# Performance work log

Measured on AMD Instinct MI355X. Metric: run time of the kernel, lower is better.

The kernel has to match this reference:

```python
import jax, jax.numpy as jnp
import numpy as np

B, N, T, D, H = 8, 1000, 64, 32, 4
HD = D // H
GEN_INTERVAL = 5.0


def setup_inputs() -> dict:
    key = jax.random.key(0)
    ks = jax.random.split(key, 10)
    s = 1.0 / np.sqrt(D)
    inp = {
        "x": jax.random.normal(ks[0], (B, N, T, D), dtype=jnp.float32),
        "q_w": jax.random.uniform(ks[1], (D, D), jnp.float32, -s, s),
        "q_b": jnp.zeros((D,), jnp.float32),
        "k_w": jax.random.uniform(ks[2], (D, D), jnp.float32, -s, s),
        "k_b": jnp.zeros((D,), jnp.float32),
        "v_w": jax.random.uniform(ks[3], (D, D), jnp.float32, -s, s),
        "v_b": jnp.zeros((D,), jnp.float32),
        "out_w": jax.random.uniform(ks[4], (D, D), jnp.float32, -s, s),
        "out_b": jnp.zeros((D,), jnp.float32),
        "rel_pos_bias": jax.random.uniform(ks[5], (H, T, T), jnp.float32, -s, s),
        "log_gi": jnp.array(np.log(GEN_INTERVAL), jnp.float32),
    }
    return inp


def _gi_mask(log_gi, t):
    # generation-interval weighting: gaussian around gen_int + recency term, causal
    gen_int = jnp.exp(log_gi)
    times = jnp.arange(t, dtype=jnp.float32)
    lag = times[:, None] - times[None, :]  # [T, T]
    weight = jnp.exp(-0.5 * ((lag - gen_int) / (gen_int * 0.5)) ** 2)
    recent = jnp.exp(-0.1 * jnp.abs(lag))
    mask = 0.7 * weight + 0.3 * recent
    causal = jnp.tril(jnp.ones((t, t), jnp.float32))
    return mask * causal


def reference(x, q_w, q_b, k_w, k_b, v_w, v_b, out_w, out_b, rel_pos_bias, log_gi):
    b, n, t, d = x.shape
    xf = x.reshape(b * n, t, d)
    q = (xf @ q_w + q_b).reshape(b * n, t, H, HD).transpose(0, 2, 1, 3)  # [BN,H,T,hd]
    k = (xf @ k_w + k_b).reshape(b * n, t, H, HD).transpose(0, 2, 1, 3)
    v = (xf @ v_w + v_b).reshape(b * n, t, H, HD).transpose(0, 2, 1, 3)
    scale = jnp.sqrt(jnp.asarray(HD, jnp.float32))
    attn = jnp.einsum("bhqd,bhkd->bhqk", q, k) / scale  # [BN,H,T,T]
    attn = attn + rel_pos_bias[None]
    gi = _gi_mask(log_gi, t)
    attn = attn * gi[None, None]
    attn = jax.nn.softmax(attn, axis=-1)
    out = jnp.einsum("bhqk,bhkd->bhqd", attn, v)
    out = out.transpose(0, 2, 1, 3).reshape(b * n, t, d)
    out = out @ out_w + out_b
    return out.reshape(b, n, t, d)
```

## Files before the change

kernel.cpp:

```cpp
#include <hip/hip_runtime.h>
#include <math.h>

namespace {
constexpr int T_ = 64;
constexpr int D_ = 32;

typedef _Float16 half4 __attribute__((ext_vector_type(4)));
typedef _Float16 half8 __attribute__((ext_vector_type(8)));
typedef float f32x4 __attribute__((ext_vector_type(4)));

__global__ __launch_bounds__(256) void gia_prep(
    const float* __restrict__ qw, const float* __restrict__ kw,
    const float* __restrict__ vw, const float* __restrict__ ow,
    const float* __restrict__ rel, const float* __restrict__ lgi,
    _Float16* __restrict__ tbl, _Float16* __restrict__ wimg)
{
    int t = blockIdx.x * 256 + threadIdx.x;
    if (t < 4096) {
        const float gv = __expf(lgi[0]);
        const float LOG2E = 1.4426950408889634f;
        const float INVS  = 0.35355339059327373f;
        int h = t >> 10, nt = (t >> 8) & 3, mt = (t >> 6) & 3, lane = t & 63;
        int q  = (lane & 15) + 16 * nt;
        int k0 = 16 * mt + 4 * (lane >> 4);
        _Float16 vals[8];
#pragma unroll
        for (int r = 0; r < 4; ++r) {
            int k = k0 + r;
            float lag = (float)(q - k);
            float gi = 0.0f;
            if (k <= q) {
                float z = (lag - gv) / (0.5f * gv);
                gi = 0.7f * __expf(-0.5f * z * z) + 0.3f * __expf(-0.1f * lag);
            }
            vals[r]     = (_Float16)(gi * INVS * LOG2E);
            vals[4 + r] = (_Float16)(rel[(h * 64 + q) * 64 + k] * gi * LOG2E);
        }
#pragma unroll
        for (int i = 0; i < 8; ++i) tbl[t * 8 + i] = vals[i];
    } else if (t < 6656) {
        int wi = t - 4096;
        const float* wp[4] = {qw, kw, vw, ow};
#pragma unroll
        for (int e = 0; e < 2; ++e) {
            int flat = wi * 2 + e;
            int m = flat / 1280, rem = flat % 1280;
            int c2 = rem / 40, kk = rem % 40;
            float v = (kk < 32) ? wp[m][kk * 32 + c2] : 0.0f;
            wimg[flat] = (_Float16)v;
        }
    }
}

__global__ __launch_bounds__(256) void gia_main(
    const float* __restrict__ x,
    const float* __restrict__ qb_, const float* __restrict__ kb_,
    const float* __restrict__ vb_, const float* __restrict__ ob_,
    const _Float16* __restrict__ tbl, const _Float16* __restrict__ wimg,
    float* __restrict__ out)
{
    __shared__ __align__(16) _Float16 xs[64][40];
    __shared__ __align__(16) _Float16 wS[4][32][40];
    __shared__ __align__(16) _Float16 qs[64][36];
    __shared__ __align__(16) _Float16 ks_[64][36];
    __shared__ __align__(16) _Float16 vT[32][72];
    __shared__ __align__(16) _Float16 os_[64][40];
    __shared__ float bS[4][32];

    const int tid  = threadIdx.x;
    const int lane = tid & 63;
    const int w    = tid >> 6;
    const int l4   = lane & 15;
    const int g    = lane >> 4;
    const int bn   = blockIdx.x;

    {
        const float4* xv = (const float4*)(x + (size_t)bn * 2048);
        float4 a = xv[2 * tid], b = xv[2 * tid + 1];
        int t = tid >> 2, c = (tid & 3) * 8;
        half8 hx;
        hx[0] = (_Float16)a.x; hx[1] = (_Float16)a.y;
        hx[2] = (_Float16)a.z; hx[3] = (_Float16)a.w;
        hx[4] = (_Float16)b.x; hx[5] = (_Float16)b.y;
        hx[6] = (_Float16)b.z; hx[7] = (_Float16)b.w;
        *(half8*)&xs[t][c] = hx;

        const uint4* wsrc = (const uint4*)wimg;
        uint4* wdst = (uint4*)&wS[0][0][0];
        wdst[tid]        = wsrc[tid];
        wdst[tid + 256]  = wsrc[tid + 256];
        if (tid < 128) wdst[tid + 512] = wsrc[tid + 512];
        if (tid < 128) {
            int m = tid >> 5, i = tid & 31;
            const float* bp = (m == 0) ? qb_ : (m == 1) ? kb_ : (m == 2) ? vb_ : ob_;
            bS[m][i] = bp[i];
        }
    }
    __syncthreads();

    {
        half4 xa0 = *(const half4*)&xs[16 * w + l4][4 * g];
        half4 xa1 = *(const half4*)&xs[16 * w + l4][4 * g + 16];
#pragma unroll
        for (int m = 0; m < 3; ++m) {
#pragma unroll
            for (int nt = 0; nt < 2; ++nt) {
                half4 wb0 = *(const half4*)&wS[m][l4 + 16 * nt][4 * g];
                half4 wb1 = *(const half4*)&wS[m][l4 + 16 * nt][4 * g + 16];
                f32x4 acc = {};
                acc = __builtin_amdgcn_mfma_f32_16x16x16f16(xa0, wb0, acc, 0, 0, 0);
                acc = __builtin_amdgcn_mfma_f32_16x16x16f16(xa1, wb1, acc, 0, 0, 0);
                float bb = bS[m][l4 + 16 * nt];
                if (m == 0) {
#pragma unroll
                    for (int r = 0; r < 4; ++r)
                        qs[g * 4 + r + 16 * w][l4 + 16 * nt] = (_Float16)(acc[r] + bb);
                } else if (m == 1) {
#pragma unroll
                    for (int r = 0; r < 4; ++r)
                        ks_[g * 4 + r + 16 * w][l4 + 16 * nt] = (_Float16)(acc[r] + bb);
                } else {
                    half4 pv;
#pragma unroll
                    for (int r = 0; r < 4; ++r) pv[r] = (_Float16)(acc[r] + bb);
                    *(half4*)&vT[l4 + 16 * nt][g * 4 + 16 * w] = pv;
                }
            }
        }
    }
    __syncthreads();

    {
        const int h = w;
        half4 kfr[4], qfr[4], vfr[4];
#pragma unroll
        for (int mt = 0; mt < 4; ++mt) {
            half4 v = {};
            if (g < 2) v = *(const half4*)&ks_[l4 + 16 * mt][8 * h + 4 * g];
            kfr[mt] = v;
        }
#pragma unroll
        for (int nt = 0; nt < 4; ++nt) {
            half4 v = {};
            if (g < 2) v = *(const half4*)&qs[l4 + 16 * nt][8 * h + 4 * g];
            qfr[nt] = v;
        }
#pragma unroll
        for (int ks = 0; ks < 4; ++ks) {
            half4 v = {};
            if (l4 < 8) v = *(const half4*)&vT[8 * h + l4][4 * g + 16 * ks];
            vfr[ks] = v;
        }

        f32x4 oacc[4];
#pragma unroll
        for (int i = 0; i < 4; ++i) oacc[i] = (f32x4){};

        const half8* tbl8 = (const half8*)tbl;
#pragma unroll
        for (int nt = 0; nt < 4; ++nt) {
            half8 tb[4];
#pragma unroll
            for (int mt = 0; mt < 4; ++mt)
                tb[mt] = tbl8[((h * 4 + nt) * 4 + mt) * 64 + lane];
            f32x4 s[4];
#pragma unroll
            for (int mt = 0; mt < 4; ++mt) {
                f32x4 z = {};
                s[mt] = __builtin_amdgcn_mfma_f32_16x16x16f16(kfr[mt], qfr[nt], z, 0, 0, 0);
            }
            float p[16];
#pragma unroll
            for (int mt = 0; mt < 4; ++mt)
#pragma unroll
                for (int r = 0; r < 4; ++r)
                    p[mt * 4 + r] =
                        fmaf(s[mt][r], (float)tb[mt][r], (float)tb[mt][4 + r]);
            float mx = p[0];
#pragma unroll
            for (int i = 1; i < 16; ++i) mx = fmaxf(mx, p[i]);
            mx = fmaxf(mx, __shfl_xor(mx, 16));
            mx = fmaxf(mx, __shfl_xor(mx, 32));
            float sum = 0.0f;
#pragma unroll
            for (int i = 0; i < 16; ++i) {
                float e = exp2f(p[i] - mx);
                p[i] = e;
                sum += e;
            }
            sum += __shfl_xor(sum, 16);
            sum += __shfl_xor(sum, 32);
            float inv = 1.0f / sum;
#pragma unroll
            for (int ks = 0; ks < 4; ++ks) {
                half4 af;
                af[0] = (_Float16)(p[ks * 4 + 0] * inv);
                af[1] = (_Float16)(p[ks * 4 + 1] * inv);
                af[2] = (_Float16)(p[ks * 4 + 2] * inv);
                af[3] = (_Float16)(p[ks * 4 + 3] * inv);
                oacc[nt] = __builtin_amdgcn_mfma_f32_16x16x16f16(af, vfr[ks], oacc[nt], 0, 0, 0);
            }
        }
        if (l4 < 8) {
#pragma unroll
            for (int nt = 0; nt < 4; ++nt)
#pragma unroll
                for (int r = 0; r < 4; ++r)
                    os_[g * 4 + r + 16 * nt][8 * h + l4] = (_Float16)oacc[nt][r];
        }
    }
    __syncthreads();

    {
        half4 oa0 = *(const half4*)&os_[16 * w + l4][4 * g];
        half4 oa1 = *(const half4*)&os_[16 * w + l4][4 * g + 16];
        float* yout = out + (size_t)bn * 2048;
#pragma unroll
        for (int nt = 0; nt < 2; ++nt) {
            half4 wb0 = *(const half4*)&wS[3][l4 + 16 * nt][4 * g];
            half4 wb1 = *(const half4*)&wS[3][l4 + 16 * nt][4 * g + 16];
            f32x4 y = {};
            y = __builtin_amdgcn_mfma_f32_16x16x16f16(oa0, wb0, y, 0, 0, 0);
            y = __builtin_amdgcn_mfma_f32_16x16x16f16(oa1, wb1, y, 0, 0, 0);
            float bb = bS[3][l4 + 16 * nt];
#pragma unroll
            for (int r = 0; r < 4; ++r)
                yout[(g * 4 + r + 16 * w) * 32 + l4 + 16 * nt] = y[r] + bb;
        }
    }
}

}

extern "C" void kernel_launch(void* const* d_in, const int* in_sizes, int n_in,
                              void* d_out, int out_size, void* d_ws, size_t ws_size,
                              hipStream_t stream)
{
    const float* x   = (const float*)d_in[0];
    const float* qw  = (const float*)d_in[1];
    const float* qb  = (const float*)d_in[2];
    const float* kw  = (const float*)d_in[3];
    const float* kb  = (const float*)d_in[4];
    const float* vw  = (const float*)d_in[5];
    const float* vb  = (const float*)d_in[6];
    const float* ow  = (const float*)d_in[7];
    const float* ob  = (const float*)d_in[8];
    const float* rel = (const float*)d_in[9];
    const float* lgi = (const float*)d_in[10];
    float* outp = (float*)d_out;

    _Float16* tbl  = (_Float16*)d_ws;
    _Float16* wimg = tbl + 32768;

    const int bn_count = in_sizes[0] / (T_ * D_);

    gia_prep<<<dim3(26), dim3(256), 0, stream>>>(qw, kw, vw, ow, rel, lgi, tbl, wimg);
    gia_main<<<dim3(bn_count), dim3(256), 0, stream>>>(
        x, qb, kb, vb, ob, tbl, wimg, outp);
}
```

Baseline: 76.41 us.

## Factor softmax exponent, drop max subtraction, and get row sums from ones column

The softmax is rewritten without max subtraction. exp(s*g + b*g) is split into exp2 of the score times a per-position fp32 gate table, multiplied by a precomputed fp16 exp(bias*gate) table. A ones row is appended to each head's V slice so the PV MFMA also produces the row sum. Normalization is then applied to the head outputs just before the output projection. This removes the per-row max/sum shuffle reductions and the division inside the attention loop, and reuses the x buffer as the output staging area. The trade-off is possible fp16 overflow if scores grow large, since there is no max subtraction.

```diff
diff --git a/kernel.cpp b/kernel.cpp
--- a/kernel.cpp
+++ b/kernel.cpp
@@ -5,47 +5,63 @@
 constexpr int T_ = 64;
 constexpr int D_ = 32;
 
+typedef _Float16 half2 __attribute__((ext_vector_type(2)));
 typedef _Float16 half4 __attribute__((ext_vector_type(4)));
 typedef _Float16 half8 __attribute__((ext_vector_type(8)));
 typedef float f32x4 __attribute__((ext_vector_type(4)));
+
+union H4 { half4 v4; half2 v2[2]; };
 
 __global__ __launch_bounds__(256) void gia_prep(
     const float* __restrict__ qw, const float* __restrict__ kw,
     const float* __restrict__ vw, const float* __restrict__ ow,
     const float* __restrict__ rel, const float* __restrict__ lgi,
-    _Float16* __restrict__ tbl, _Float16* __restrict__ wimg)
+    float* __restrict__ gis32, _Float16* __restrict__ ebg,
+    _Float16* __restrict__ wimg)
 {
     int t = blockIdx.x * 256 + threadIdx.x;
-    if (t < 4096) {
-        const float gv = __expf(lgi[0]);
-        const float LOG2E = 1.4426950408889634f;
-        const float INVS  = 0.35355339059327373f;
-        int h = t >> 10, nt = (t >> 8) & 3, mt = (t >> 6) & 3, lane = t & 63;
+    const float gv = __expf(lgi[0]);
+    const float LOG2E = 1.4426950408889634f;
+    const float INVS  = 0.35355339059327373f;
+    if (t < 1024) {
+        int nt = t >> 8, mt = (t >> 6) & 3, lane = t & 63;
         int q  = (lane & 15) + 16 * nt;
         int k0 = 16 * mt + 4 * (lane >> 4);
-        _Float16 vals[8];
 #pragma unroll
         for (int r = 0; r < 4; ++r) {
             int k = k0 + r;
-            float lag = (float)(q - k);
             float gi = 0.0f;
             if (k <= q) {
+                float lag = (float)(q - k);
                 float z = (lag - gv) / (0.5f * gv);
                 gi = 0.7f * __expf(-0.5f * z * z) + 0.3f * __expf(-0.1f * lag);
             }
-            vals[r]     = (_Float16)(gi * INVS * LOG2E);
-            vals[4 + r] = (_Float16)(rel[(h * 64 + q) * 64 + k] * gi * LOG2E);
-        }
-#pragma unroll
-        for (int i = 0; i < 8; ++i) tbl[t * 8 + i] = vals[i];
-    } else if (t < 6656) {
-        int wi = t - 4096;
+            gis32[t * 4 + r] = gi * INVS * LOG2E;
+        }
+    } else if (t < 5120) {
+        int e = t - 1024;
+        int h = e >> 10, nt = (e >> 8) & 3, mt = (e >> 6) & 3, lane = e & 63;
+        int q  = (lane & 15) + 16 * nt;
+        int k0 = 16 * mt + 4 * (lane >> 4);
+#pragma unroll
+        for (int r = 0; r < 4; ++r) {
+            int k = k0 + r;
+            float gi = 0.0f;
+            if (k <= q) {
+                float lag = (float)(q - k);
+                float z = (lag - gv) / (0.5f * gv);
+                gi = 0.7f * __expf(-0.5f * z * z) + 0.3f * __expf(-0.1f * lag);
+            }
+            ebg[e * 4 + r] = (_Float16)__expf(rel[(h * 64 + q) * 64 + k] * gi);
+        }
+    } else if (t < 7424) {
+        int wi = t - 5120;
         const float* wp[4] = {qw, kw, vw, ow};
 #pragma unroll
         for (int e = 0; e < 2; ++e) {
             int flat = wi * 2 + e;
-            int m = flat / 1280, rem = flat % 1280;
-            int c2 = rem / 40, kk = rem % 40;
+            int m = flat / 1152, rem = flat % 1152;
+            int c2 = rem / 36, kk = rem % 36;
             float v = (kk < 32) ? wp[m][kk * 32 + c2] : 0.0f;
             wimg[flat] = (_Float16)v;
         }
@@ -56,16 +72,17 @@
     const float* __restrict__ x,
     const float* __restrict__ qb_, const float* __restrict__ kb_,
     const float* __restrict__ vb_, const float* __restrict__ ob_,
-    const _Float16* __restrict__ tbl, const _Float16* __restrict__ wimg,
+    const float* __restrict__ gis32, const _Float16* __restrict__ ebg,
+    const _Float16* __restrict__ wimg,
     float* __restrict__ out)
 {
     __shared__ __align__(16) _Float16 xs[64][40];
-    __shared__ __align__(16) _Float16 wS[4][32][40];
-    __shared__ __align__(16) _Float16 qs[64][36];
-    __shared__ __align__(16) _Float16 ks_[64][36];
-    __shared__ __align__(16) _Float16 vT[32][72];
-    __shared__ __align__(16) _Float16 os_[64][40];
+    __shared__ __align__(16) _Float16 wS[4][32][36];
+    __shared__ __align__(16) _Float16 qs[64][40];
+    __shared__ __align__(16) _Float16 ks_[64][40];
+    __shared__ __align__(16) _Float16 vT[37][72];
     __shared__ float bS[4][32];
+    __shared__ float invS[4][64];
 
     const int tid  = threadIdx.x;
     const int lane = tid & 63;
@@ -87,9 +104,15 @@
 
         const uint4* wsrc = (const uint4*)wimg;
         uint4* wdst = (uint4*)&wS[0][0][0];
-        wdst[tid]        = wsrc[tid];
-        wdst[tid + 256]  = wsrc[tid + 256];
-        if (tid < 128) wdst[tid + 512] = wsrc[tid + 512];
+        wdst[tid]       = wsrc[tid];
+        wdst[tid + 256] = wsrc[tid + 256];
+        if (tid < 64) wdst[tid + 512] = wsrc[tid + 512];
+
+        if (tid < 128) {
+            int h = tid >> 5, j = tid & 31;
+            half2 o2 = {(_Float16)1.0f, (_Float16)1.0f};
+            *(half2*)&vT[9 * h + 8][2 * j] = o2;
+        }
         if (tid < 128) {
             int m = tid >> 5, i = tid & 31;
             const float* bp = (m == 0) ? qb_ : (m == 1) ? kb_ : (m == 2) ? vb_ : ob_;
@@ -123,7 +146,8 @@
                     half4 pv;
 #pragma unroll
                     for (int r = 0; r < 4; ++r) pv[r] = (_Float16)(acc[r] + bb);
-                    *(half4*)&vT[l4 + 16 * nt][g * 4 + 16 * w] = pv;
+                    int c = l4 + 16 * nt;
+                    *(half4*)&vT[9 * (c >> 3) + (c & 7)][g * 4 + 16 * w] = pv;
                 }
             }
         }
@@ -145,75 +169,68 @@
             if (g < 2) v = *(const half4*)&qs[l4 + 16 * nt][8 * h + 4 * g];
             qfr[nt] = v;
         }
-#pragma unroll
-        for (int ks = 0; ks < 4; ++ks) {
-            half4 v = {};
-            if (l4 < 8) v = *(const half4*)&vT[8 * h + l4][4 * g + 16 * ks];
-            vfr[ks] = v;
-        }
+        const int vrow = 9 * h + (l4 < 9 ? l4 : 9);
+#pragma unroll
+        for (int ks = 0; ks < 4; ++ks)
+            vfr[ks] = *(const half4*)&vT[vrow][4 * g + 16 * ks];
 
         f32x4 oacc[4];
 #pragma unroll
         for (int i = 0; i < 4; ++i) oacc[i] = (f32x4){};
 
-        const half8* tbl8 = (const half8*)tbl;
 #pragma unroll
         for (int nt = 0; nt < 4; ++nt) {
-            half8 tb[4];
-#pragma unroll
-            for (int mt = 0; mt < 4; ++mt)
-                tb[mt] = tbl8[((h * 4 + nt) * 4 + mt) * 64 + lane];
             f32x4 s[4];
 #pragma unroll
             for (int mt = 0; mt < 4; ++mt) {
                 f32x4 z = {};
                 s[mt] = __builtin_amdgcn_mfma_f32_16x16x16f16(kfr[mt], qfr[nt], z, 0, 0, 0);
             }
-            float p[16];
-#pragma unroll
-            for (int mt = 0; mt < 4; ++mt)
-#pragma unroll
-                for (int r = 0; r < 4; ++r)
-                    p[mt * 4 + r] =
-                        fmaf(s[mt][r], (float)tb[mt][r], (float)tb[mt][4 + r]);
-            float mx = p[0];
-#pragma unroll
-            for (int i = 1; i < 16; ++i) mx = fmaxf(mx, p[i]);
-            mx = fmaxf(mx, __shfl_xor(mx, 16));
-            mx = fmaxf(mx, __shfl_xor(mx, 32));
-            float sum = 0.0f;
-#pragma unroll
-            for (int i = 0; i < 16; ++i) {
-                float e = exp2f(p[i] - mx);
-                p[i] = e;
-                sum += e;
-            }
-            sum += __shfl_xor(sum, 16);
-            sum += __shfl_xor(sum, 32);
-            float inv = 1.0f / sum;
-#pragma unroll
-            for (int ks = 0; ks < 4; ++ks) {
-                half4 af;
-                af[0] = (_Float16)(p[ks * 4 + 0] * inv);
-                af[1] = (_Float16)(p[ks * 4 + 1] * inv);
-                af[2] = (_Float16)(p[ks * 4 + 2] * inv);
-                af[3] = (_Float16)(p[ks * 4 + 3] * inv);
-                oacc[nt] = __builtin_amdgcn_mfma_f32_16x16x16f16(af, vfr[ks], oacc[nt], 0, 0, 0);
-            }
-        }
+            half4 af[4];
+#pragma unroll
+            for (int mt = 0; mt < 4; ++mt) {
+                f32x4 g4 = *(const f32x4*)&gis32[((nt * 4 + mt) * 64 + lane) * 4];
+                half4 eb = *(const half4*)&ebg[(((h * 4 + nt) * 4 + mt) * 64 + lane) * 4];
+                float t0 = s[mt][0] * g4[0];
+                float t1 = s[mt][1] * g4[1];
+                float t2 = s[mt][2] * g4[2];
+                float t3 = s[mt][3] * g4[3];
+                H4 u;
+                u.v2[0] = __builtin_bit_cast(half2, __builtin_amdgcn_cvt_pkrtz(exp2f(t0), exp2f(t1)));
+                u.v2[1] = __builtin_bit_cast(half2, __builtin_amdgcn_cvt_pkrtz(exp2f(t2), exp2f(t3)));
+                af[mt] = u.v4 * eb;
+            }
+#pragma unroll
+            for (int ks = 0; ks < 4; ++ks)
+                oacc[nt] = __builtin_amdgcn_mfma_f32_16x16x16f16(af[ks], vfr[ks], oacc[nt], 0, 0, 0);
+        }
+
+        _Float16 (*os_)[40] = xs;
         if (l4 < 8) {
 #pragma unroll
             for (int nt = 0; nt < 4; ++nt)
 #pragma unroll
                 for (int r = 0; r < 4; ++r)
                     os_[g * 4 + r + 16 * nt][8 * h + l4] = (_Float16)oacc[nt][r];
+        } else if (l4 == 8) {
+#pragma unroll
+            for (int nt = 0; nt < 4; ++nt)
+#pragma unroll
+                for (int r = 0; r < 4; ++r)
+                    invS[h][g * 4 + r + 16 * nt] = oacc[nt][r];
         }
     }
     __syncthreads();
 
     {
+        _Float16 (*os_)[40] = xs;
         half4 oa0 = *(const half4*)&os_[16 * w + l4][4 * g];
         half4 oa1 = *(const half4*)&os_[16 * w + l4][4 * g + 16];
+        float i0 = 1.0f / invS[g >> 1][16 * w + l4];
+        float i1 = 1.0f / invS[2 + (g >> 1)][16 * w + l4];
+        _Float16 h0 = (_Float16)i0, h1 = (_Float16)i1;
+        oa0 *= (half4){h0, h0, h0, h0};
+        oa1 *= (half4){h1, h1, h1, h1};
         float* yout = out + (size_t)bn * 2048;
 #pragma unroll
         for (int nt = 0; nt < 2; ++nt) {
@@ -249,12 +266,14 @@
     const float* lgi = (const float*)d_in[10];
     float* outp = (float*)d_out;
 
-    _Float16* tbl  = (_Float16*)d_ws;
-    _Float16* wimg = tbl + 32768;
+    float*    gis32 = (float*)d_ws;
+    _Float16* ebg   = (_Float16*)((char*)d_ws + 16384);
+    _Float16* wimg  = (_Float16*)((char*)d_ws + 49152);
 
     const int bn_count = in_sizes[0] / (T_ * D_);
 
-    gia_prep<<<dim3(26), dim3(256), 0, stream>>>(qw, kw, vw, ow, rel, lgi, tbl, wimg);
+    gia_prep<<<dim3(29), dim3(256), 0, stream>>>(qw, kw, vw, ow, rel, lgi,
+                                                 gis32, ebg, wimg);
     gia_main<<<dim3(bn_count), dim3(256), 0, stream>>>(
-        x, qb, kb, vb, ob, tbl, wimg, outp);
-}
+        x, qb, kb, vb, ob, gis32, ebg, wimg, outp);
+}
```

Result: faster. 66.14 us (-13.4%).
